# Performance work log

Measured on AMD Instinct MI355X. Metric: run time of the kernel, lower is better.

Reference implementation:

```python
import jax, jax.numpy as jnp
import numpy as np

N_TOKENS = 4096   # flattened batch*seq tokens
D_MODEL = 1024
N_EXPERT = 8
D_HIDDEN = 1024   # expert FFN hidden size
TOP_K = 2


def setup_inputs() -> dict:
    key = jax.random.key(0)
    ks = jax.random.split(key, 4)
    f32 = jnp.float32
    return {
        "inp": jax.random.normal(ks[0], (N_TOKENS, D_MODEL), f32),
        "gate_w": jax.random.normal(ks[1], (D_MODEL, N_EXPERT), f32) * 0.02,
        "gate_b": jnp.zeros((N_EXPERT,), f32),
        "w1": jax.random.normal(ks[2], (N_EXPERT, D_MODEL, D_HIDDEN), f32) * 0.02,
        "b1": jnp.zeros((N_EXPERT, D_HIDDEN), f32),
        "w2": jax.random.normal(ks[3], (N_EXPERT, D_HIDDEN, D_MODEL), f32) * 0.02,
        "b2": jnp.zeros((N_EXPERT, D_MODEL), f32),
    }


def reference(inp, gate_w, gate_b, w1, b1, w2, b2):
    """FMoE forward: NaiveGate top-k -> dispatch -> per-expert FFN -> weighted combine.

    Math is identical to dispatch/grouped-GEMM/gather: since both top-k slots of a
    token see the same input, out[n] = sum_e coeff[n,e] * expert_e(inp[n]) where
    coeff[n,e] = sum_k softmax(top_vals)[n,k] * 1[top_idx[n,k] == e].
    """
    n_expert = gate_w.shape[-1]
    # NaiveGate: linear gate, top-k, softmax over the k selected logits
    logits = inp @ gate_w + gate_b                      # [N, E]
    top_val, top_idx = jax.lax.top_k(logits, TOP_K)     # [N, K]
    score = jax.nn.softmax(top_val, axis=-1)            # [N, K]
    # combine weights per (token, expert); top-k indices are distinct per token
    coeff = jnp.sum(
        jax.nn.one_hot(top_idx, n_expert, dtype=inp.dtype) * score[..., None],
        axis=1,
    )                                                   # [N, E]
    # expert FFN (exact-erf GeLU, matching torch.nn.functional.gelu)
    h = jax.nn.gelu(jnp.einsum('nd,edh->neh', inp, w1) + b1, approximate=False)  # [N, E, H]
    out = jnp.einsum('neh,ehd->nd', h * coeff[:, :, None], w2) + coeff @ b2      # [N, D]
    return out


if __name__ == "__main__":
    out = reference(**setup_inputs())
    print(out.shape, out.dtype)
```

## Files before the change

### kernel.cpp

```cpp
#include <hip/hip_runtime.h>
#include <math.h>

#define N_TOKENS 4096
#define D_MODEL  1024
#define N_EXPERT 8
#define D_HIDDEN 1024
#define N_POS    8192

typedef __bf16 bf16x8 __attribute__((ext_vector_type(8)));
typedef float  f32x4  __attribute__((ext_vector_type(4)));
typedef unsigned short u16x8 __attribute__((ext_vector_type(8)));

#define GLOBAL_AS __attribute__((address_space(1)))
#define LDS_AS    __attribute__((address_space(3)))

static __device__ __forceinline__ void async_ld16(const void* g, void* l) {
    __builtin_amdgcn_global_load_lds((GLOBAL_AS void*)g, (LDS_AS void*)l, 16, 0, 0);
}

static __device__ __forceinline__ unsigned short f2bf(float f) {
    unsigned int u = __builtin_bit_cast(unsigned int, f);
    u += 0x7fffu + ((u >> 16) & 1u);
    return (unsigned short)(u >> 16);
}
static __device__ __forceinline__ unsigned int pack2(float a, float b) {
    return (unsigned int)f2bf(a) | ((unsigned int)f2bf(b) << 16);
}
static __device__ __forceinline__ float bflo(unsigned int u) {
    return __builtin_bit_cast(float, u << 16);
}
static __device__ __forceinline__ float bfhi(unsigned int u) {
    return __builtin_bit_cast(float, u & 0xffff0000u);
}

__global__ __launch_bounds__(256) void convert_transpose_kernel(
    const float* __restrict__ w1, const float* __restrict__ w2,
    unsigned short* __restrict__ w1b, unsigned short* __restrict__ w2b)
{
    int mat = blockIdx.z;
    const float* src = (mat < 8) ? (w1 + (size_t)mat * 1048576)
                                 : (w2 + (size_t)(mat - 8) * 1048576);
    unsigned short* dst = (mat < 8) ? (w1b + (size_t)mat * 1048576)
                                    : (w2b + (size_t)(mat - 8) * 1048576);
    __shared__ float tile[64][68];
    int r0 = blockIdx.x * 64, c0 = blockIdx.y * 64;
    int tid = threadIdx.x;
    #pragma unroll
    for (int i = 0; i < 4; ++i) {
        int r = (tid >> 4) + i * 16;
        float4 v = *(const float4*)(src + (size_t)(r0 + r) * 1024 + c0 + (tid & 15) * 4);
        *(float4*)&tile[r][(tid & 15) * 4] = v;
    }
    __syncthreads();
    int dr = tid >> 2;
    #pragma unroll
    for (int p = 0; p < 2; ++p) {
        int ch = (tid & 3) + p * 4;
        u16x8 o;
        #pragma unroll
        for (int j = 0; j < 8; ++j) o[j] = f2bf(tile[ch * 8 + j][dr]);
        *(u16x8*)(dst + (size_t)(c0 + dr) * 1024 + r0 + ch * 8) = o;
    }
}

__global__ __launch_bounds__(256) void gate_kernel(
    const float* __restrict__ inp, const float* __restrict__ gate_w,
    const float* __restrict__ gate_b, int* __restrict__ cnts,
    int* __restrict__ emeta, float* __restrict__ stok)
{
    __shared__ int bcnt[8], base[8];
    __shared__ int tinfo[16];
    int tid = threadIdx.x, lane = tid & 63, wave = tid >> 6;
    if (tid < 8) bcnt[tid] = 0;
    __syncthreads();

    for (int t = 0; t < 4; ++t) {
        int ti = wave * 4 + t;
        int n  = blockIdx.x * 16 + ti;
        const float* ip = inp + (size_t)n * D_MODEL;
        float acc[8] = {0.f,0.f,0.f,0.f,0.f,0.f,0.f,0.f};
        for (int d0 = lane * 4; d0 < D_MODEL; d0 += 256) {
            float4 x = *(const float4*)(ip + d0);
            #pragma unroll
            for (int j = 0; j < 4; ++j) {
                float xv = (j == 0) ? x.x : (j == 1) ? x.y : (j == 2) ? x.z : x.w;
                float4 g0 = *(const float4*)(gate_w + (d0 + j) * 8);
                float4 g1 = *(const float4*)(gate_w + (d0 + j) * 8 + 4);
                acc[0] += xv * g0.x; acc[1] += xv * g0.y;
                acc[2] += xv * g0.z; acc[3] += xv * g0.w;
                acc[4] += xv * g1.x; acc[5] += xv * g1.y;
                acc[6] += xv * g1.z; acc[7] += xv * g1.w;
            }
        }
        #pragma unroll
        for (int off = 32; off > 0; off >>= 1)
            #pragma unroll
            for (int e = 0; e < 8; ++e)
                acc[e] += __shfl_xor(acc[e], off, 64);
        #pragma unroll
        for (int e = 0; e < 8; ++e) acc[e] += gate_b[e];

        int e0 = 0; float v0 = acc[0];
        #pragma unroll
        for (int e = 1; e < 8; ++e) if (acc[e] > v0) { v0 = acc[e]; e0 = e; }
        int e1 = -1; float v1 = -1e30f;
        #pragma unroll
        for (int e = 0; e < 8; ++e) if (e != e0 && acc[e] > v1) { v1 = acc[e]; e1 = e; }
        float tv = expf(v1 - v0);
        float s0 = 1.0f / (1.0f + tv);
        float s1 = tv / (1.0f + tv);

        if (lane == 0) {
            int r0 = atomicAdd(&bcnt[e0], 1);
            int r1 = atomicAdd(&bcnt[e1], 1);
            tinfo[ti] = e0 | (e1 << 4) | (r0 << 8) | (r1 << 20);
            stok[2 * n]     = s0;
            stok[2 * n + 1] = s1;
        }
    }
    __syncthreads();
    if (tid < 8) base[tid] = atomicAdd(&cnts[tid], bcnt[tid]);
    __syncthreads();
    if (tid < 16) {
        int n = blockIdx.x * 16 + tid;
        unsigned int inf = (unsigned int)tinfo[tid];
        int e0 = inf & 15, e1 = (inf >> 4) & 15;
        int p0 = base[e0] + ((inf >> 8) & 4095);
        int p1 = base[e1] + (int)(inf >> 20);
        emeta[n] = e0 | (e1 << 4) | (p0 << 8) | (p1 << 20);
    }
}

__global__ __launch_bounds__(256) void gather_kernel(
    const float* __restrict__ inp, const int* __restrict__ cnts,
    const int* __restrict__ emeta, unsigned short* __restrict__ Ag,
    int* __restrict__ tok2pos)
{
    int lane = threadIdx.x & 63, wave = threadIdx.x >> 6;
    int n = blockIdx.x * 4 + wave;
    unsigned int em = (unsigned int)emeta[n];
    int e0 = em & 15, e1 = (em >> 4) & 15;
    int p0 = (em >> 8) & 4095, p1 = (int)(em >> 20);
    int off0 = 0, off1 = 0;
    #pragma unroll
    for (int e = 0; e < 8; ++e) {
        int c = cnts[e];
        off0 += (e < e0) ? c : 0;
        off1 += (e < e1) ? c : 0;
    }
    int pos0 = off0 + p0, pos1 = off1 + p1;
    if (lane == 0) {
        tok2pos[2 * n]     = pos0;
        tok2pos[2 * n + 1] = pos1;
    }
    const float* ip = inp + (size_t)n * D_MODEL;
    unsigned short* r0 = Ag + (size_t)pos0 * D_MODEL;
    unsigned short* r1 = Ag + (size_t)pos1 * D_MODEL;
    for (int d = lane * 4; d < D_MODEL; d += 256) {
        float4 v = *(const float4*)(ip + d);
        uint2 u; u.x = pack2(v.x, v.y); u.y = pack2(v.z, v.w);
        *(uint2*)(r0 + d) = u;
        *(uint2*)(r1 + d) = u;
    }
}

__global__ __launch_bounds__(256, 2) void ffn1_kernel(
    const unsigned short* __restrict__ Ag, const unsigned short* __restrict__ w1b,
    const float* __restrict__ b1, const int* __restrict__ cnts,
    unsigned short* __restrict__ Hg)
{
    int bid = blockIdx.x;
    int e = bid & 7, nt = (bid >> 3) & 7, mt = bid >> 6;
    int off = 0, Ne = 0;
    #pragma unroll
    for (int i = 0; i < 8; ++i) {
        int c = cnts[i];
        off += (i < e) ? c : 0;
        Ne = (i == e) ? c : Ne;
    }
    int m0 = mt * 128;
    if (m0 >= Ne) return;
    int n0 = nt * 128;

    __shared__ unsigned short As[2 * 128 * 32];
    __shared__ unsigned short Bs[2 * 128 * 32];

    int tid = threadIdx.x, lane = tid & 63, wave = tid >> 6;
    int lrow = lane >> 2, lchunk = lane & 3;
    int csw8 = (lchunk ^ ((lrow >> 1) & 3)) * 8;

    int ga0 = off + m0 + wave * 32 + lrow;
    int ga1 = ga0 + 16;
    if (ga0 >= N_POS) ga0 = N_POS - 1;
    if (ga1 >= N_POS) ga1 = N_POS - 1;
    const unsigned short* aS0 = Ag + (size_t)ga0 * D_MODEL + csw8;
    const unsigned short* aS1 = Ag + (size_t)ga1 * D_MODEL + csw8;
    const unsigned short* bS0 = w1b + (size_t)e * D_MODEL * D_HIDDEN
                              + (size_t)(n0 + wave * 32 + lrow) * D_MODEL + csw8;
    const unsigned short* bS1 = bS0 + (size_t)16 * D_MODEL;
    unsigned short* aD0 = &As[(wave * 32) * 32];
    unsigned short* aD1 = &As[(wave * 32 + 16) * 32];
    unsigned short* bD0 = &Bs[(wave * 32) * 32];
    unsigned short* bD1 = &Bs[(wave * 32 + 16) * 32];

    f32x4 acc[4][4] = {};
    int wm = (wave & 1) * 64, wn = (wave >> 1) * 64;
    int lane15 = lane & 15, quad = lane >> 4;
    int fro = (quad ^ ((lane15 >> 1) & 3)) * 8;

    for (int k0 = 0; k0 < D_MODEL; k0 += 64) {
        #pragma unroll
        for (int h = 0; h < 2; ++h) {
            int ko = k0 + h * 32;
            async_ld16(aS0 + ko, aD0 + h * 4096);
            async_ld16(aS1 + ko, aD1 + h * 4096);
            async_ld16(bS0 + ko, bD0 + h * 4096);
            async_ld16(bS1 + ko, bD1 + h * 4096);
        }
        __syncthreads();
        bf16x8 af[2][4], bf[2][4];
        #pragma unroll
        for (int h = 0; h < 2; ++h)
            #pragma unroll
            for (int t = 0; t < 4; ++t) {
                af[h][t] = *(const bf16x8*)&As[h * 4096 + (wm + t * 16 + lane15) * 32 + fro];
                bf[h][t] = *(const bf16x8*)&Bs[h * 4096 + (wn + t * 16 + lane15) * 32 + fro];
            }
        #pragma unroll
        for (int h = 0; h < 2; ++h)
            #pragma unroll
            for (int i = 0; i < 4; ++i)
                #pragma unroll
                for (int j = 0; j < 4; ++j)
                    acc[i][j] = __builtin_amdgcn_mfma_f32_16x16x32_bf16(
                        af[h][i], bf[h][j], acc[i][j], 0, 0, 0);
        __syncthreads();
    }

    const float* bexp = b1 + (size_t)e * D_HIDDEN;
    #pragma unroll
    for (int j = 0; j < 4; ++j) {
        int gcol = n0 + wn + j * 16 + lane15;
        float bv = bexp[gcol];
        #pragma unroll
        for (int i = 0; i < 4; ++i) {
            int rowb = wm + i * 16 + quad * 4;
            #pragma unroll
            for (int r = 0; r < 4; ++r) {
                int row = rowb + r;
                if (m0 + row < Ne) {
                    float x = acc[i][j][r] + bv;
                    float gv = 0.5f * x * (1.0f + erff(x * 0.70710678118654752f));
                    Hg[(size_t)(off + m0 + row) * D_HIDDEN + gcol] = f2bf(gv);
                }
            }
        }
    }
}

__global__ __launch_bounds__(256, 2) void ffn2_kernel(
    const unsigned short* __restrict__ Hg, const unsigned short* __restrict__ w2b,
    const int* __restrict__ cnts, unsigned short* __restrict__ Og)
{
    int bid = blockIdx.x;
    int e = bid & 7, nt = (bid >> 3) & 7, mt = bid >> 6;
    int off = 0, Ne = 0;
    #pragma unroll
    for (int i = 0; i < 8; ++i) {
        int c = cnts[i];
        off += (i < e) ? c : 0;
        Ne = (i == e) ? c : Ne;
    }
    int m0 = mt * 128;
    if (m0 >= Ne) return;
    int n0 = nt * 128;

    __shared__ unsigned short As[2 * 128 * 32];
    __shared__ unsigned short Bs[2 * 128 * 32];

    int tid = threadIdx.x, lane = tid & 63, wave = tid >> 6;
    int lrow = lane >> 2, lchunk = lane & 3;
    int csw8 = (lchunk ^ ((lrow >> 1) & 3)) * 8;

    int ga0 = off + m0 + wave * 32 + lrow;
    int ga1 = ga0 + 16;
    if (ga0 >= N_POS) ga0 = N_POS - 1;
    if (ga1 >= N_POS) ga1 = N_POS - 1;
    const unsigned short* aS0 = Hg + (size_t)ga0 * D_HIDDEN + csw8;
    const unsigned short* aS1 = Hg + (size_t)ga1 * D_HIDDEN + csw8;
    const unsigned short* bS0 = w2b + (size_t)e * D_HIDDEN * D_MODEL
                              + (size_t)(n0 + wave * 32 + lrow) * D_HIDDEN + csw8;
    const unsigned short* bS1 = bS0 + (size_t)16 * D_HIDDEN;
    unsigned short* aD0 = &As[(wave * 32) * 32];
    unsigned short* aD1 = &As[(wave * 32 + 16) * 32];
    unsigned short* bD0 = &Bs[(wave * 32) * 32];
    unsigned short* bD1 = &Bs[(wave * 32 + 16) * 32];

    f32x4 acc[4][4] = {};
    int wm = (wave & 1) * 64, wn = (wave >> 1) * 64;
    int lane15 = lane & 15, quad = lane >> 4;
    int fro = (quad ^ ((lane15 >> 1) & 3)) * 8;

    for (int k0 = 0; k0 < D_HIDDEN; k0 += 64) {
        #pragma unroll
        for (int h = 0; h < 2; ++h) {
            int ko = k0 + h * 32;
            async_ld16(aS0 + ko, aD0 + h * 4096);
            async_ld16(aS1 + ko, aD1 + h * 4096);
            async_ld16(bS0 + ko, bD0 + h * 4096);
            async_ld16(bS1 + ko, bD1 + h * 4096);
        }
        __syncthreads();
        bf16x8 af[2][4], bf[2][4];
        #pragma unroll
        for (int h = 0; h < 2; ++h)
            #pragma unroll
            for (int t = 0; t < 4; ++t) {
                af[h][t] = *(const bf16x8*)&As[h * 4096 + (wm + t * 16 + lane15) * 32 + fro];
                bf[h][t] = *(const bf16x8*)&Bs[h * 4096 + (wn + t * 16 + lane15) * 32 + fro];
            }
        #pragma unroll
        for (int h = 0; h < 2; ++h)
            #pragma unroll
            for (int i = 0; i < 4; ++i)
                #pragma unroll
                for (int j = 0; j < 4; ++j)
                    acc[i][j] = __builtin_amdgcn_mfma_f32_16x16x32_bf16(
                        af[h][i], bf[h][j], acc[i][j], 0, 0, 0);
        __syncthreads();
    }

    #pragma unroll
    for (int j = 0; j < 4; ++j) {
        int gcol = n0 + wn + j * 16 + lane15;
        #pragma unroll
        for (int i = 0; i < 4; ++i) {
            int rowb = wm + i * 16 + quad * 4;
            #pragma unroll
            for (int r = 0; r < 4; ++r) {
                int row = rowb + r;
                if (m0 + row < Ne) {
                    Og[(size_t)(off + m0 + row) * D_MODEL + gcol] =
                        f2bf(acc[i][j][r]);
                }
            }
        }
    }
}

__global__ __launch_bounds__(256) void combine_kernel(
    const unsigned short* __restrict__ Og, const int* __restrict__ tok2pos,
    const float* __restrict__ stok, const int* __restrict__ emeta,
    const float* __restrict__ b2, float* __restrict__ out)
{
    int lane = threadIdx.x & 63, wave = threadIdx.x >> 6;
    int n = blockIdx.x * 4 + wave;
    int pos0 = tok2pos[2 * n], pos1 = tok2pos[2 * n + 1];
    float s0 = stok[2 * n], s1 = stok[2 * n + 1];
    unsigned int em = (unsigned int)emeta[n];
    int e0 = em & 15, e1 = (em >> 4) & 15;
    const unsigned short* o0 = Og + (size_t)pos0 * D_MODEL;
    const unsigned short* o1 = Og + (size_t)pos1 * D_MODEL;
    const float* bA = b2 + (size_t)e0 * D_MODEL;
    const float* bB = b2 + (size_t)e1 * D_MODEL;
    float* op = out + (size_t)n * D_MODEL;
    for (int d = lane * 4; d < D_MODEL; d += 256) {
        uint2 u0 = *(const uint2*)(o0 + d);
        uint2 u1 = *(const uint2*)(o1 + d);
        float4 xa = *(const float4*)(bA + d);
        float4 xb = *(const float4*)(bB + d);
        float4 r;
        r.x = s0 * (bflo(u0.x) + xa.x) + s1 * (bflo(u1.x) + xb.x);
        r.y = s0 * (bfhi(u0.x) + xa.y) + s1 * (bfhi(u1.x) + xb.y);
        r.z = s0 * (bflo(u0.y) + xa.z) + s1 * (bflo(u1.y) + xb.z);
        r.w = s0 * (bfhi(u0.y) + xa.w) + s1 * (bfhi(u1.y) + xb.w);
        *(float4*)(op + d) = r;
    }
}

extern "C" void kernel_launch(void* const* d_in, const int* in_sizes, int n_in,
                              void* d_out, int out_size, void* d_ws, size_t ws_size,
                              hipStream_t stream) {
    const float* inp    = (const float*)d_in[0];
    const float* gate_w = (const float*)d_in[1];
    const float* gate_b = (const float*)d_in[2];
    const float* w1     = (const float*)d_in[3];
    const float* b1     = (const float*)d_in[4];
    const float* w2     = (const float*)d_in[5];
    const float* b2     = (const float*)d_in[6];
    float* out = (float*)d_out;

    char* ws = (char*)d_ws;
    int*   cnts    = (int*)  (ws);
    int*   emeta   = (int*)  (ws + 4096);
    float* stok    = (float*)(ws + 65536);
    int*   tok2pos = (int*)  (ws + 131072);
    unsigned short* w2b = (unsigned short*)(ws + 1048576);
    unsigned short* Hg  = (unsigned short*)(ws + 17825792);
    unsigned short* w1b = (unsigned short*)(ws + 34603008);
    unsigned short* Og  = (unsigned short*)(ws + 34603008);

    unsigned short* Ag = (unsigned short*)d_out;

    hipMemsetAsync(cnts, 0, N_EXPERT * sizeof(int), stream);
    convert_transpose_kernel<<<dim3(16, 16, 16), 256, 0, stream>>>(w1, w2, w1b, w2b);
    gate_kernel<<<dim3(N_TOKENS / 16), 256, 0, stream>>>(
        inp, gate_w, gate_b, cnts, emeta, stok);
    gather_kernel<<<dim3(N_TOKENS / 4), 256, 0, stream>>>(
        inp, cnts, emeta, Ag, tok2pos);
    ffn1_kernel<<<dim3(2048), 256, 0, stream>>>(Ag, w1b, b1, cnts, Hg);
    ffn2_kernel<<<dim3(2048), 256, 0, stream>>>(Hg, w2b, cnts, Og);
    combine_kernel<<<dim3(N_TOKENS / 4), 256, 0, stream>>>(
        Og, tok2pos, stok, emeta, b2, out);
}
```

Baseline: 227.7 us.

## Restructure expert GEMMs as weight-stationary LDS slabs with direct-global A streaming

```diff
diff --git a/kernel.cpp b/kernel.cpp
--- a/kernel.cpp
+++ b/kernel.cpp
@@ -35,8 +35,12 @@
 
 __global__ __launch_bounds__(256) void convert_transpose_kernel(
     const float* __restrict__ w1, const float* __restrict__ w2,
-    unsigned short* __restrict__ w1b, unsigned short* __restrict__ w2b)
-{
+    unsigned short* __restrict__ w1b, unsigned short* __restrict__ w2b,
+    int* __restrict__ cnts)
+{
+    int tid = threadIdx.x;
+    if (blockIdx.x == 0 && blockIdx.y == 0 && blockIdx.z == 0 && tid < 8)
+        cnts[tid] = 0;
     int mat = blockIdx.z;
     const float* src = (mat < 8) ? (w1 + (size_t)mat * 1048576)
                                  : (w2 + (size_t)(mat - 8) * 1048576);
@@ -44,7 +48,6 @@
                                     : (w2b + (size_t)(mat - 8) * 1048576);
     __shared__ float tile[64][68];
     int r0 = blockIdx.x * 64, c0 = blockIdx.y * 64;
-    int tid = threadIdx.x;
     #pragma unroll
     for (int i = 0; i < 4; ++i) {
         int r = (tid >> 4) + i * 16;
@@ -164,13 +167,14 @@
     }
 }
 
-__global__ __launch_bounds__(256, 2) void ffn1_kernel(
-    const unsigned short* __restrict__ Ag, const unsigned short* __restrict__ w1b,
-    const float* __restrict__ b1, const int* __restrict__ cnts,
-    unsigned short* __restrict__ Hg)
+template <bool GELU>
+__device__ __forceinline__ void ffn_gemm(
+    const unsigned short* __restrict__ A, const unsigned short* __restrict__ Bw,
+    const float* __restrict__ bias, const int* __restrict__ cnts,
+    unsigned short* __restrict__ Out)
 {
     int bid = blockIdx.x;
-    int e = bid & 7, nt = (bid >> 3) & 7, mt = bid >> 6;
+    int e = bid & 7, nt = (bid >> 3) & 15, ms = bid >> 7;
     int off = 0, Ne = 0;
     #pragma unroll
     for (int i = 0; i < 8; ++i) {
@@ -178,174 +182,116 @@
         off += (i < e) ? c : 0;
         Ne = (i == e) ? c : Ne;
     }
-    int m0 = mt * 128;
-    if (m0 >= Ne) return;
-    int n0 = nt * 128;
-
-    __shared__ unsigned short As[2 * 128 * 32];
-    __shared__ unsigned short Bs[2 * 128 * 32];
+    int n0 = nt * 64;
+
+    __shared__ unsigned short Bs[64 * 1024];
 
     int tid = threadIdx.x, lane = tid & 63, wave = tid >> 6;
-    int lrow = lane >> 2, lchunk = lane & 3;
-    int csw8 = (lchunk ^ ((lrow >> 1) & 3)) * 8;
-
-    int ga0 = off + m0 + wave * 32 + lrow;
-    int ga1 = ga0 + 16;
-    if (ga0 >= N_POS) ga0 = N_POS - 1;
-    if (ga1 >= N_POS) ga1 = N_POS - 1;
-    const unsigned short* aS0 = Ag + (size_t)ga0 * D_MODEL + csw8;
-    const unsigned short* aS1 = Ag + (size_t)ga1 * D_MODEL + csw8;
-    const unsigned short* bS0 = w1b + (size_t)e * D_MODEL * D_HIDDEN
-                              + (size_t)(n0 + wave * 32 + lrow) * D_MODEL + csw8;
-    const unsigned short* bS1 = bS0 + (size_t)16 * D_MODEL;
-    unsigned short* aD0 = &As[(wave * 32) * 32];
-    unsigned short* aD1 = &As[(wave * 32 + 16) * 32];
-    unsigned short* bD0 = &Bs[(wave * 32) * 32];
-    unsigned short* bD1 = &Bs[(wave * 32 + 16) * 32];
-
-    f32x4 acc[4][4] = {};
-    int wm = (wave & 1) * 64, wn = (wave >> 1) * 64;
     int lane15 = lane & 15, quad = lane >> 4;
-    int fro = (quad ^ ((lane15 >> 1) & 3)) * 8;
-
-    for (int k0 = 0; k0 < D_MODEL; k0 += 64) {
-        #pragma unroll
-        for (int h = 0; h < 2; ++h) {
-            int ko = k0 + h * 32;
-            async_ld16(aS0 + ko, aD0 + h * 4096);
-            async_ld16(aS1 + ko, aD1 + h * 4096);
-            async_ld16(bS0 + ko, bD0 + h * 4096);
-            async_ld16(bS1 + ko, bD1 + h * 4096);
-        }
-        __syncthreads();
-        bf16x8 af[2][4], bf[2][4];
-        #pragma unroll
-        for (int h = 0; h < 2; ++h)
-            #pragma unroll
-            for (int t = 0; t < 4; ++t) {
-                af[h][t] = *(const bf16x8*)&As[h * 4096 + (wm + t * 16 + lane15) * 32 + fro];
-                bf[h][t] = *(const bf16x8*)&Bs[h * 4096 + (wn + t * 16 + lane15) * 32 + fro];
+
+    const unsigned short* bsrc = Bw + (size_t)e * 1024 * 1024;
+    #pragma unroll
+    for (int t = 0; t < 16; ++t) {
+        int idx = wave * 16 + t;
+        int col = idx >> 1;
+        int sbase = (idx & 1) * 64;
+        int cc = (sbase + lane) ^ (col & 7);
+        async_ld16(bsrc + (size_t)(n0 + col) * 1024 + cc * 8,
+                   &Bs[(size_t)(col * 128 + sbase) * 8]);
+    }
+    __syncthreads();
+
+    float bv[4];
+    if (GELU) {
+        #pragma unroll
+        for (int j = 0; j < 4; ++j)
+            bv[j] = bias[e * 1024 + n0 + j * 16 + lane15];
+    }
+
+    for (int g = ms * 8 + wave; g * 64 < Ne; g += 16) {
+        const unsigned short* ap[4];
+        #pragma unroll
+        for (int i = 0; i < 4; ++i) {
+            int rr = g * 64 + i * 16 + lane15;
+            if (rr >= Ne) rr = Ne - 1;
+            ap[i] = A + (size_t)(off + rr) * 1024 + quad * 8;
+        }
+
+        f32x4 acc[4][4] = {};
+        bf16x8 av[4], bw[4];
+        #pragma unroll
+        for (int i = 0; i < 4; ++i) av[i] = *(const bf16x8*)(ap[i]);
+        #pragma unroll
+        for (int j = 0; j < 4; ++j) {
+            int col = j * 16 + lane15;
+            bw[j] = *(const bf16x8*)&Bs[col * 1024 + ((quad ^ (col & 7)) << 3)];
+        }
+
+        for (int k0 = 0; k0 < 1024; k0 += 32) {
+            bf16x8 an[4], bn[4];
+            bool more = (k0 + 32) < 1024;
+            if (more) {
+                #pragma unroll
+                for (int i = 0; i < 4; ++i)
+                    an[i] = *(const bf16x8*)(ap[i] + k0 + 32);
+                #pragma unroll
+                for (int j = 0; j < 4; ++j) {
+                    int col = j * 16 + lane15;
+                    int cc = ((k0 + 32) >> 3) + quad;
+                    bn[j] = *(const bf16x8*)
+                        &Bs[col * 1024 + ((cc ^ (col & 7)) << 3)];
+                }
             }
-        #pragma unroll
-        for (int h = 0; h < 2; ++h)
             #pragma unroll
             for (int i = 0; i < 4; ++i)
                 #pragma unroll
                 for (int j = 0; j < 4; ++j)
                     acc[i][j] = __builtin_amdgcn_mfma_f32_16x16x32_bf16(
-                        af[h][i], bf[h][j], acc[i][j], 0, 0, 0);
-        __syncthreads();
-    }
-
-    const float* bexp = b1 + (size_t)e * D_HIDDEN;
-    #pragma unroll
-    for (int j = 0; j < 4; ++j) {
-        int gcol = n0 + wn + j * 16 + lane15;
-        float bv = bexp[gcol];
-        #pragma unroll
-        for (int i = 0; i < 4; ++i) {
-            int rowb = wm + i * 16 + quad * 4;
+                        av[i], bw[j], acc[i][j], 0, 0, 0);
+            if (more) {
+                #pragma unroll
+                for (int i = 0; i < 4; ++i) av[i] = an[i];
+                #pragma unroll
+                for (int j = 0; j < 4; ++j) bw[j] = bn[j];
+            }
+        }
+
+        #pragma unroll
+        for (int j = 0; j < 4; ++j) {
+            int gcol = n0 + j * 16 + lane15;
             #pragma unroll
-            for (int r = 0; r < 4; ++r) {
-                int row = rowb + r;
-                if (m0 + row < Ne) {
-                    float x = acc[i][j][r] + bv;
-                    float gv = 0.5f * x * (1.0f + erff(x * 0.70710678118654752f));
-                    Hg[(size_t)(off + m0 + row) * D_HIDDEN + gcol] = f2bf(gv);
+            for (int i = 0; i < 4; ++i) {
+                int rowb = g * 64 + i * 16 + quad * 4;
+                #pragma unroll
+                for (int r = 0; r < 4; ++r) {
+                    int row = rowb + r;
+                    if (row < Ne) {
+                        float x = acc[i][j][r];
+                        if (GELU) {
+                            x += bv[j];
+                            x = 0.5f * x * (1.0f + erff(x * 0.70710678118654752f));
+                        }
+                        Out[(size_t)(off + row) * 1024 + gcol] = f2bf(x);
+                    }
                 }
             }
         }
     }
 }
 
-__global__ __launch_bounds__(256, 2) void ffn2_kernel(
+__global__ __launch_bounds__(512, 2) void ffn1_kernel(
+    const unsigned short* __restrict__ Ag, const unsigned short* __restrict__ w1b,
+    const float* __restrict__ b1, const int* __restrict__ cnts,
+    unsigned short* __restrict__ Hg)
+{
+    ffn_gemm<true>(Ag, w1b, b1, cnts, Hg);
+}
+
+__global__ __launch_bounds__(512, 2) void ffn2_kernel(
     const unsigned short* __restrict__ Hg, const unsigned short* __restrict__ w2b,
     const int* __restrict__ cnts, unsigned short* __restrict__ Og)
 {
-    int bid = blockIdx.x;
-    int e = bid & 7, nt = (bid >> 3) & 7, mt = bid >> 6;
-    int off = 0, Ne = 0;
-    #pragma unroll
-    for (int i = 0; i < 8; ++i) {
-        int c = cnts[i];
-        off += (i < e) ? c : 0;
-        Ne = (i == e) ? c : Ne;
-    }
-    int m0 = mt * 128;
-    if (m0 >= Ne) return;
-    int n0 = nt * 128;
-
-    __shared__ unsigned short As[2 * 128 * 32];
-    __shared__ unsigned short Bs[2 * 128 * 32];
-
-    int tid = threadIdx.x, lane = tid & 63, wave = tid >> 6;
-    int lrow = lane >> 2, lchunk = lane & 3;
-    int csw8 = (lchunk ^ ((lrow >> 1) & 3)) * 8;
-
-    int ga0 = off + m0 + wave * 32 + lrow;
-    int ga1 = ga0 + 16;
-    if (ga0 >= N_POS) ga0 = N_POS - 1;
-    if (ga1 >= N_POS) ga1 = N_POS - 1;
-    const unsigned short* aS0 = Hg + (size_t)ga0 * D_HIDDEN + csw8;
-    const unsigned short* aS1 = Hg + (size_t)ga1 * D_HIDDEN + csw8;
-    const unsigned short* bS0 = w2b + (size_t)e * D_HIDDEN * D_MODEL
-                              + (size_t)(n0 + wave * 32 + lrow) * D_HIDDEN + csw8;
-    const unsigned short* bS1 = bS0 + (size_t)16 * D_HIDDEN;
-    unsigned short* aD0 = &As[(wave * 32) * 32];
-    unsigned short* aD1 = &As[(wave * 32 + 16) * 32];
-    unsigned short* bD0 = &Bs[(wave * 32) * 32];
-    unsigned short* bD1 = &Bs[(wave * 32 + 16) * 32];
-
-    f32x4 acc[4][4] = {};
-    int wm = (wave & 1) * 64, wn = (wave >> 1) * 64;
-    int lane15 = lane & 15, quad = lane >> 4;
-    int fro = (quad ^ ((lane15 >> 1) & 3)) * 8;
-
-    for (int k0 = 0; k0 < D_HIDDEN; k0 += 64) {
-        #pragma unroll
-        for (int h = 0; h < 2; ++h) {
-            int ko = k0 + h * 32;
-            async_ld16(aS0 + ko, aD0 + h * 4096);
-            async_ld16(aS1 + ko, aD1 + h * 4096);
-            async_ld16(bS0 + ko, bD0 + h * 4096);
-            async_ld16(bS1 + ko, bD1 + h * 4096);
-        }
-        __syncthreads();
-        bf16x8 af[2][4], bf[2][4];
-        #pragma unroll
-        for (int h = 0; h < 2; ++h)
-            #pragma unroll
-            for (int t = 0; t < 4; ++t) {
-                af[h][t] = *(const bf16x8*)&As[h * 4096 + (wm + t * 16 + lane15) * 32 + fro];
-                bf[h][t] = *(const bf16x8*)&Bs[h * 4096 + (wn + t * 16 + lane15) * 32 + fro];
-            }
-        #pragma unroll
-        for (int h = 0; h < 2; ++h)
-            #pragma unroll
-            for (int i = 0; i < 4; ++i)
-                #pragma unroll
-                for (int j = 0; j < 4; ++j)
-                    acc[i][j] = __builtin_amdgcn_mfma_f32_16x16x32_bf16(
-                        af[h][i], bf[h][j], acc[i][j], 0, 0, 0);
-        __syncthreads();
-    }
-
-    #pragma unroll
-    for (int j = 0; j < 4; ++j) {
-        int gcol = n0 + wn + j * 16 + lane15;
-        #pragma unroll
-        for (int i = 0; i < 4; ++i) {
-            int rowb = wm + i * 16 + quad * 4;
-            #pragma unroll
-            for (int r = 0; r < 4; ++r) {
-                int row = rowb + r;
-                if (m0 + row < Ne) {
-                    Og[(size_t)(off + m0 + row) * D_MODEL + gcol] =
-                        f2bf(acc[i][j][r]);
-                }
-            }
-        }
-    }
+    ffn_gemm<false>(Hg, w2b, nullptr, cnts, Og);
 }
 
 __global__ __launch_bounds__(256) void combine_kernel(
@@ -402,14 +348,14 @@
 
     unsigned short* Ag = (unsigned short*)d_out;
 
-    hipMemsetAsync(cnts, 0, N_EXPERT * sizeof(int), stream);
-    convert_transpose_kernel<<<dim3(16, 16, 16), 256, 0, stream>>>(w1, w2, w1b, w2b);
+    convert_transpose_kernel<<<dim3(16, 16, 16), 256, 0, stream>>>(
+        w1, w2, w1b, w2b, cnts);
     gate_kernel<<<dim3(N_TOKENS / 16), 256, 0, stream>>>(
         inp, gate_w, gate_b, cnts, emeta, stok);
     gather_kernel<<<dim3(N_TOKENS / 4), 256, 0, stream>>>(
         inp, cnts, emeta, Ag, tok2pos);
-    ffn1_kernel<<<dim3(2048), 256, 0, stream>>>(Ag, w1b, b1, cnts, Hg);
-    ffn2_kernel<<<dim3(2048), 256, 0, stream>>>(Hg, w2b, cnts, Og);
+    ffn1_kernel<<<dim3(256), 512, 0, stream>>>(Ag, w1b, b1, cnts, Hg);
+    ffn2_kernel<<<dim3(256), 512, 0, stream>>>(Hg, w2b, cnts, Og);
     combine_kernel<<<dim3(N_TOKENS / 4), 256, 0, stream>>>(
         Og, tok2pos, stok, emeta, b2, out);
 }
```

Result: slower. 462.9 us (+103.3%).
